# Kernel optimization log

Measured on AMD Instinct MI355X. Metric: run time of the kernel, lower is better.

Reference implementation:

```python
import math
import jax, jax.numpy as jnp
import numpy as np

E = 1024          # emb_size
H = 16            # num_heads
D = E // H        # head_dim
B, S = 4, 2048
DI = 64           # intent dim
K = 32            # num intent clusters
ASSIGN_W = 0.5
MU_W = 0.5
UNC_W = 0.5
EXPLORE_SCALE = 0.5
EXPLOIT_SCALE = 0.5
TEMP_MIN = 0.5
TEMP_MAX = 2.0


def setup_inputs() -> dict:
    key = jax.random.key(0)
    ks = jax.random.split(key, 16)
    inp = {
        "his_emb": jax.random.normal(ks[0], (B, S, E), dtype=jnp.float32),
        "src_key_padding_mask": jax.random.randint(ks[1], (B, S), 0, 2).astype(bool),
        "intent_mu": jax.random.normal(ks[2], (B, S, DI), dtype=jnp.float32),
        "intent_sigma": jax.random.uniform(ks[3], (B, S, DI), dtype=jnp.float32),
        "intent_assign": jax.random.uniform(ks[4], (B, S, K), dtype=jnp.float32),
        "explore": jax.random.uniform(ks[5], (B, S), dtype=jnp.float32),
        "exploit": jax.random.uniform(ks[6], (B, S), dtype=jnp.float32),
    }
    std = 0.02
    inp["Wq"] = jax.random.normal(ks[7], (E, E), dtype=jnp.float32) * std
    inp["bq"] = jnp.zeros((E,), dtype=jnp.float32)
    inp["Wk"] = jax.random.normal(ks[8], (E, E), dtype=jnp.float32) * std
    inp["bk"] = jnp.zeros((E,), dtype=jnp.float32)
    inp["Wv"] = jax.random.normal(ks[9], (E, E), dtype=jnp.float32) * std
    inp["bv"] = jnp.zeros((E,), dtype=jnp.float32)
    inp["Wo"] = jax.random.normal(ks[10], (E, E), dtype=jnp.float32) * std
    inp["bo"] = jnp.zeros((E,), dtype=jnp.float32)
    return inp


def _forward(his_emb, src_key_padding_mask, intent_mu, intent_sigma, intent_assign,
             explore, exploit, Wq, bq, Wk, bk, Wv, bv, Wo, bo):
    b, s, _ = his_emb.shape
    # projections -> [b, h, s, d]
    def proj(W, bias):
        return (his_emb @ W.T + bias).reshape(b, s, H, D).transpose(0, 2, 1, 3)
    q, k, v = proj(Wq, bq), proj(Wk, bk), proj(Wv, bv)

    logits = jnp.einsum("bhqd,bhkd->bhqk", q, k) / math.sqrt(D)  # [b,h,s,s]

    # intent bias [b, s, s]
    assign_sim = jnp.einsum("bqc,bkc->bqk", intent_assign, intent_assign)
    bias = ASSIGN_W * assign_sim
    # mean squared distance via expansion (avoids [b,s,s,DI] intermediate)
    sq = jnp.sum(intent_mu * intent_mu, axis=-1)  # [b,s]
    dot = jnp.einsum("bqd,bkd->bqk", intent_mu, intent_mu)
    mu_dist = (sq[:, :, None] + sq[:, None, :] - 2.0 * dot) / DI
    bias = bias - MU_W * mu_dist
    uncertainty = jnp.mean(intent_sigma, axis=-1)[:, None, :]  # [b,1,s] over keys
    bias = bias - UNC_W * uncertainty

    logits = logits + bias[:, None, :, :]

    attn_mask = src_key_padding_mask[:, None, None, :]  # [b,1,1,s]
    logits = jnp.where(attn_mask, -1e16, logits)

    # per-query temperature scaling
    temperature = 1.0 + EXPLORE_SCALE * explore - EXPLOIT_SCALE * exploit
    temperature = jnp.clip(temperature, TEMP_MIN, TEMP_MAX)
    temperature = jnp.where(src_key_padding_mask, 1.0, temperature)  # [b,s]
    logits = logits / temperature[:, None, :, None]

    probs = jax.nn.softmax(logits, axis=-1)
    probs = jnp.where(attn_mask, 0.0, probs)
    probs = probs / jnp.maximum(jnp.sum(probs, axis=-1, keepdims=True), 1e-8)

    out = jnp.einsum("bhqk,bhkd->bhqd", probs, v)
    out = out.transpose(0, 2, 1, 3).reshape(b, s, E)
    out = out @ Wo.T + bo
    return jnp.where(src_key_padding_mask[:, :, None], 0.0, out)


def reference(his_emb, src_key_padding_mask, intent_mu, intent_sigma, intent_assign,
              explore, exploit, Wq, bq, Wk, bk, Wv, bv, Wo, bo):
    return _forward(his_emb, src_key_padding_mask, intent_mu, intent_sigma,
                    intent_assign, explore, exploit, Wq, bq, Wk, bk, Wv, bv, Wo, bo)
```

## Files before the change

kernel.cpp:

```cpp
#include <hip/hip_runtime.h>
#include <hip/hip_bf16.h>
#include <stdint.h>
#include <stddef.h>

#define Bn 4
#define Sn 2048
#define En 1024
#define Hn 16
#define DIn 64
#define BSn (Bn*Sn)
#define L2E 1.44269504089f
#define SH8L 11.5415603271f

typedef __attribute__((ext_vector_type(8))) short short8;
typedef __attribute__((ext_vector_type(4))) short short4v;
typedef __attribute__((ext_vector_type(4))) float fx4;
typedef __attribute__((ext_vector_type(16))) float fx16;
typedef __attribute__((ext_vector_type(8))) _Float16 half8;
typedef __attribute__((ext_vector_type(2))) __fp16 fp16x2;
typedef __attribute__((ext_vector_type(4))) int ix4;

__device__ __forceinline__ short f2bf(float f){
  union U { __hip_bfloat16 h; short s; } u; u.h = __float2bfloat16(f); return u.s;
}
__device__ __forceinline__ short f2h(float f){
  _Float16 h = (_Float16)f; return __builtin_bit_cast(short, h);
}

__device__ __forceinline__ void async16(const void* g, void* l){
  __builtin_amdgcn_global_load_lds((const __attribute__((address_space(1))) unsigned int*)g,
                                   (__attribute__((address_space(3))) unsigned int*)l, 16, 0, 0);
}

__device__ __forceinline__ fx4 mfma_bf(short8 a, short8 b, fx4 c){
  return __builtin_amdgcn_mfma_f32_16x16x32_bf16(a, b, c, 0, 0, 0);
}
__device__ __forceinline__ fx4 mfma_h(short8 a, short8 b, fx4 c){
  return __builtin_amdgcn_mfma_f32_16x16x32_f16(__builtin_bit_cast(half8, a),
                                                __builtin_bit_cast(half8, b), c, 0, 0, 0);
}
__device__ __forceinline__ fx16 mfma32h(short8 a, short8 b, fx16 c){
  return __builtin_amdgcn_mfma_f32_32x32x16_f16(__builtin_bit_cast(half8, a),
                                                __builtin_bit_cast(half8, b), c, 0, 0, 0);
}

#define FENCE asm volatile("" ::: "memory")
#define WAIT_VM4 asm volatile("s_waitcnt vmcnt(4)" ::: "memory")
#define WAIT_VM8 asm volatile("s_waitcnt vmcnt(8)" ::: "memory")
#define WAIT_VM0 asm volatile("s_waitcnt vmcnt(0)" ::: "memory")
#define WAIT_LGKM0 asm volatile("s_waitcnt lgkmcnt(0)" ::: "memory")

__global__ void scan_mask_k(const int* __restrict__ mask, int* __restrict__ sidx,
                            int* __restrict__ scnt){
  int b = blockIdx.x;
  const int* mb = mask + (size_t)b*Sn;
  __shared__ int wsum[4];
  int tid = threadIdx.x;
  int v[8]; int c = 0;
  #pragma unroll
  for (int j=0;j<8;j++){ v[j] = (mb[tid*8+j] == 0); c += v[j]; }
  int lane = tid&63, wv = tid>>6;
  int pref = c;
  #pragma unroll
  for (int m=1; m<64; m<<=1){ int o = __shfl_up(pref, m, 64); if (lane >= m) pref += o; }
  if (lane==63) wsum[wv] = pref;
  __syncthreads();
  int wbase = 0;
  for (int wprev=0; wprev<wv; wprev++) wbase += wsum[wprev];
  int pos = wbase + pref - c;
  #pragma unroll
  for (int j=0;j<8;j++){ if (v[j]) sidx[(size_t)b*Sn + pos++] = tid*8+j; }
  if (tid==255) scnt[b] = wbase + pref;
}

__global__ void prep_rows_k(const float* __restrict__ mu, const float* __restrict__ sigma,
                            const float* __restrict__ assign, const float* __restrict__ explore,
                            const float* __restrict__ exploit, const int* __restrict__ mask,
                            _Float16* __restrict__ F, _Float16* __restrict__ G,
                            float* __restrict__ a1L){
  int r = blockIdx.x*4 + (threadIdx.x>>6);
  int lane = threadIdx.x & 63;
  float muv = mu[(size_t)r*DIn + lane];
  float sgv = sigma[(size_t)r*DIn + lane];
  float sq = muv*muv, sg = sgv;
  #pragma unroll
  for (int m=32; m; m>>=1){ sq += __shfl_xor(sq,m,64); sg += __shfl_xor(sg,m,64); }
  float unc = sg*(1.f/64.f);
  #pragma unroll
  for (int cb=0; cb<128; cb+=64){
    int col = cb + lane;
    float fv, gv;
    if (col < 32){ float a = assign[(size_t)r*32 + col]; fv = 0.5f*a; gv = a; }
    else if (col < 96){ float m2 = mu[(size_t)r*DIn + (col-32)]; fv = m2*(1.f/64.f); gv = m2; }
    else if (col == 96){ fv = -sq*(1.f/128.f); gv = 1.f; }
    else if (col == 97){ fv = 1.f; gv = -(sq*(1.f/128.f) + 0.5f*unc); }
    else { fv = 0.f; gv = 0.f; }
    F[(size_t)r*128 + col] = (_Float16)fv;
    G[(size_t)r*128 + col] = (_Float16)gv;
  }
  if (lane == 0){
    int mk = mask[r];
    float t = 1.f + 0.5f*explore[r] - 0.5f*exploit[r];
    t = fminf(fmaxf(t, 0.5f), 2.f);
    if (mk) t = 1.f;
    a1L[r] = 0.125f/t * L2E;
  }
}

__global__ __launch_bounds__(256) void gather_x_k(
    const float* __restrict__ his, const int* __restrict__ sidx, const int* __restrict__ scnt,
    const float* __restrict__ a1L, short* __restrict__ Xc, float* __restrict__ a1Lc)
{
  int b = blockIdx.y, jb = blockIdx.x;
  int cnt = scnt[b];
  int scp = (cnt + 127) & ~127;
  int j0 = jb*64;
  if (j0 >= scp) return;
  __shared__ int sj[64];
  int tid = threadIdx.x;
  if (tid < 64){
    int j = j0 + tid;
    int s = (j < cnt) ? sidx[(size_t)b*Sn + j] : -1;
    sj[tid] = s;
    a1Lc[(size_t)b*Sn + j] = (s >= 0) ? a1L[(size_t)b*Sn + s] : 1.0f;
  }
  __syncthreads();
  const float* hb = his + (size_t)b*Sn*En;
  short* Xb_ = Xc + ((size_t)b*Sn + j0)*En;
  #pragma unroll 4
  for (int it=0; it<64; it++){
    int i = it*256 + tid;
    int r = i>>8, c = i&255;
    int s = sj[r];
    short4v o;
    if (s >= 0){
      fx4 v = *(const fx4*)(hb + (size_t)s*En + c*4);
      o = (short4v){ f2bf(v[0]), f2bf(v[1]), f2bf(v[2]), f2bf(v[3]) };
    } else o = (short4v){0,0,0,0};
    *(short4v*)(Xb_ + (size_t)r*En + c*4) = o;
  }
}

__global__ void cast_w_k(const float* __restrict__ Wq, const float* __restrict__ Wk,
                         const float* __restrict__ Wv, const float* __restrict__ Wo,
                         short* __restrict__ WQKV, short* __restrict__ Wof){
  int i = blockIdx.x*256 + threadIdx.x;
  int seg = i >> 18;
  int off = i & 262143;
  const float* src = (seg==0)?Wq:(seg==1)?Wk:(seg==2)?Wv:Wo;
  fx4 v = ((const fx4*)src)[off];
  short4v o;
  if (seg < 3) o = (short4v){ f2bf(v[0]), f2bf(v[1]), f2bf(v[2]), f2bf(v[3]) };
  else         o = (short4v){ f2h(v[0]),  f2h(v[1]),  f2h(v[2]),  f2h(v[3])  };
  if (seg < 3) ((short4v*)WQKV)[(size_t)seg*262144 + off] = o;
  else         ((short4v*)Wof)[off] = o;
}

__global__ void zero_masked_k(const int* __restrict__ mask, float* __restrict__ out){
  int row = blockIdx.x;
  if (!mask[row]) return;
  fx4 z = {0.f,0.f,0.f,0.f};
  ((fx4*)(out + (size_t)row*En))[threadIdx.x] = z;
}


__global__ __launch_bounds__(256) void gemm_qkv_k(
    const short* __restrict__ A, const short* __restrict__ Wqkv,
    short* __restrict__ Q, short* __restrict__ K, short* __restrict__ Vt,
    const float* __restrict__ bq, const float* __restrict__ bk, const float* __restrict__ bv,
    const int* __restrict__ scnt)
{
  __shared__ short sm[17408];
  short* Ct = sm;
  const int tid = threadIdx.x;
  const int wv = tid>>6, lane = tid&63, quad = lane>>4, l16 = lane&15;
  const int m0 = blockIdx.y*128, n0g = blockIdx.x*128;
  const int bb = m0 >> 11, jloc = m0 & 2047;
  const int scp = (scnt[bb] + 127) & ~127;
  if (jloc >= scp) return;
  const int seg = n0g >> 10, nloc = n0g & 1023;
  const int wm = (wv>>1)*64, wn = (wv&1)*64;
  int srw[2], sgc[2];
  #pragma unroll
  for (int i=0; i<2; i++){
    int idx = i*256 + tid;
    srw[i] = 2*(idx>>3) + (idx&1);
    sgc[i] = (((idx>>1)&3) ^ ((idx>>3)&3))*8;
  }
  auto stage = [&](int kt, short* dA, short* dB){
    int k0 = kt*32;
    #pragma unroll
    for (int i=0; i<2; i++){
      int idx = i*256 + tid;
      async16(A    + (size_t)(m0+srw[i])*En  + k0 + sgc[i], dA + idx*8);
      async16(Wqkv + (size_t)(n0g+srw[i])*En + k0 + sgc[i], dB + idx*8);
    }
  };
  fx4 acc[4][4] = {};
  int roffA[4], roffB[4];
  #pragma unroll
  for (int mi=0; mi<4; mi++){
    int row = wm + mi*16 + l16;
    roffA[mi] = (row>>1)*64 + ((quad ^ ((row>>1)&3))*16) + (row&1)*8;
    int rowb = wn + mi*16 + l16;
    roffB[mi] = (rowb>>1)*64 + ((quad ^ ((rowb>>1)&3))*16) + (rowb&1)*8;
  }
  auto compute = [&](const short* cA, const short* cB){
    short8 af[4], bfr[4];
    #pragma unroll
    for (int mi=0; mi<4; mi++) af[mi]  = *(const short8*)&cA[roffA[mi]];
    #pragma unroll
    for (int ni=0; ni<4; ni++) bfr[ni] = *(const short8*)&cB[roffB[ni]];
    #pragma unroll
    for (int mi=0; mi<4; mi++)
      #pragma unroll
      for (int ni=0; ni<4; ni++)
        acc[mi][ni] = mfma_bf(af[mi], bfr[ni], acc[mi][ni]);
  };
  stage(0, sm, sm+8192);
  for (int kt2=0; kt2<16; kt2++){
    stage(2*kt2+1, sm+4096, sm+12288);
    WAIT_VM4;
    __builtin_amdgcn_s_barrier(); FENCE;
    compute(sm, sm+8192);
    WAIT_LGKM0;
    __builtin_amdgcn_s_barrier(); FENCE;
    if (kt2 < 15){ stage(2*kt2+2, sm, sm+8192); WAIT_VM4; }
    else         { WAIT_VM0; }
    __builtin_amdgcn_s_barrier(); FENCE;
    compute(sm+4096, sm+12288);
    WAIT_LGKM0;
    __builtin_amdgcn_s_barrier(); FENCE;
  }
  __syncthreads();
  const float* biasv = (seg == 0) ? bq : (seg == 1) ? bk : bv;
  if (seg < 2){
    short* C = seg ? K : Q;
    #pragma unroll
    for (int mi=0; mi<4; mi++)
      #pragma unroll
      for (int ni=0; ni<4; ni++){
        int col = nloc + wn + ni*16 + l16;
        float b0 = biasv[col];
        #pragma unroll
        for (int rg=0; rg<4; rg++){
          int row = m0 + wm + mi*16 + quad*4 + rg;
          C[(size_t)row*En + col] = f2h(acc[mi][ni][rg] + b0);
        }
      }
  } else {
    #pragma unroll
    for (int mi=0; mi<4; mi++)
      #pragma unroll
      for (int ni=0; ni<4; ni++){
        int lcol = wn + ni*16 + l16;
        int lrow = wm + mi*16 + quad*4;
        float b0 = biasv[nloc + lcol];
        short4v pk;
        #pragma unroll
        for (int rg=0; rg<4; rg++) pk[rg] = f2h(acc[mi][ni][rg] + b0);
        *(short4v*)&Ct[lcol*136 + lrow] = pk;
      }
    __syncthreads();
    int sl = (tid&15)*8;
    #pragma unroll
    for (int e8=0; e8<8; e8++){
      int e_l = e8*16 + (tid>>4);
      fx4 val = *(const fx4*)&Ct[e_l*136 + sl];
      int e_g = nloc + e_l;
      size_t dst = ((size_t)(bb*Hn + (e_g>>6))*64 + (e_g&63))*Sn + jloc + sl;
      *(fx4*)&Vt[dst] = val;
    }
  }
}

__global__ __launch_bounds__(256) void gemm_bias_k(
    const short* __restrict__ G, const short* __restrict__ F, _Float16* __restrict__ biasT,
    const float* __restrict__ a1Lc, const int* __restrict__ sidx, const int* __restrict__ scnt)
{
  __shared__ short sm[32768];
  const int tid = threadIdx.x, b = blockIdx.z;
  const int cnt = scnt[b];
  const int scp64  = (cnt + 63) & ~63;
  const int scp128 = (cnt + 127) & ~127;
  const int m0 = blockIdx.y*128, n0 = blockIdx.x*128;
  if (m0 >= scp64)  return;
  if (n0 >= scp128) return;
  const int wv = tid>>6, lane = tid&63, quad = lane>>4, l16 = lane&15;
  const int wm = (wv>>1)*64, wn = (wv&1)*64;
  const short* Gb = G + (size_t)b*Sn*128;
  const short* Fb = F + (size_t)b*Sn*128;
  const int* sx = sidx + (size_t)b*Sn;
  int rA[4], rB[4];
  #pragma unroll
  for (int i=0; i<4; i++){
    int s = i*256 + tid;
    int r = s>>3;
    int gr = m0 + r;  rA[i] = (gr < cnt) ? sx[gr] : 0;
    int qr = n0 + r;  rB[i] = (qr < cnt) ? sx[qr] : 0;
  }
  #pragma unroll
  for (int h=0; h<2; h++){
    #pragma unroll
    for (int i=0; i<4; i++){
      int s = i*256 + tid;
      int r = s>>3, cl8 = s&7;
      int cg = (h*8 + (cl8 ^ (r&7)))*8;
      async16(Gb + (size_t)rA[i]*128 + cg, &sm[h*8192 + s*8]);
      async16(Fb + (size_t)rB[i]*128 + cg, &sm[16384 + h*8192 + s*8]);
    }
  }
  fx4 acc[4][4] = {};
  #pragma unroll
  for (int h=0; h<2; h++){
    if (h == 0){ WAIT_VM8; } else { WAIT_VM0; }
    __builtin_amdgcn_s_barrier();
    FENCE;
    #pragma unroll
    for (int kk=0; kk<2; kk++){
      short8 af[4], bfr[4];
      #pragma unroll
      for (int mi=0; mi<4; mi++){
        int row = wm + mi*16 + l16, pc = (kk*4+quad) ^ (row&7);
        af[mi] = *(const short8*)&sm[h*8192 + row*64 + pc*8];
      }
      #pragma unroll
      for (int ni=0; ni<4; ni++){
        int row = wn + ni*16 + l16, pc = (kk*4+quad) ^ (row&7);
        bfr[ni] = *(const short8*)&sm[16384 + h*8192 + row*64 + pc*8];
      }
      #pragma unroll
      for (int mi=0; mi<4; mi++)
        #pragma unroll
        for (int ni=0; ni<4; ni++)
          acc[mi][ni] = mfma_h(af[mi], bfr[ni], acc[mi][ni]);
    }
  }
  _Float16* bQ = biasT + (size_t)b*Sn*Sn;
  #pragma unroll
  for (int mi=0; mi<4; mi++)
    #pragma unroll
    for (int ni=0; ni<4; ni++){
      int col = n0 + wn + ni*16 + l16;
      int rowb = m0 + wm + mi*16 + quad*4;
      float s8 = 8.f * a1Lc[b*Sn + col];
      short4v pk;
      #pragma unroll
      for (int rg=0; rg<4; rg++){
        int s = rowb + rg;
        short hv;
        if (s >= cnt) hv = (short)0xFC00;
        else hv = f2h(acc[mi][ni][rg]*s8 - SH8L);
        pk[rg] = hv;
      }
      *(short4v*)&bQ[((size_t)(rowb>>3)*Sn + col)*8 + (rowb&7)] = pk;
    }
}

__global__ __launch_bounds__(256) void gemm_out_k(
    const short* __restrict__ A, const short* __restrict__ Bm, float* __restrict__ C,
    const float* __restrict__ biasv, const int* __restrict__ sidx, const int* __restrict__ scnt)
{
  __shared__ short sm[16384];
  const int tid = threadIdx.x;
  const int wv = tid>>6, lane = tid&63, quad = lane>>4, l16 = lane&15;
  const int m0 = blockIdx.y*128, n0 = blockIdx.x*128;
  const int b = m0 >> 11, jloc = m0 & 2047;
  const int cnt = scnt[b];
  const int scp = (cnt + 127) & ~127;
  if (jloc >= scp) return;
  const int* sx = sidx + (size_t)b*Sn;
  const int wm = (wv>>1)*64, wn = (wv&1)*64;
  int srw[2], sgc[2];
  #pragma unroll
  for (int i=0; i<2; i++){
    int idx = i*256 + tid;
    srw[i] = 2*(idx>>3) + (idx&1);
    sgc[i] = (((idx>>1)&3) ^ ((idx>>3)&3))*8;
  }
  auto stage = [&](int kt, short* dA, short* dB){
    int k0 = kt*32;
    #pragma unroll
    for (int i=0; i<2; i++){
      int idx = i*256 + tid;
      async16(A  + (size_t)(m0+srw[i])*En + k0 + sgc[i], dA + idx*8);
      async16(Bm + (size_t)(n0+srw[i])*En + k0 + sgc[i], dB + idx*8);
    }
  };
  fx4 acc[4][4] = {};
  int roffA[4], roffB[4];
  #pragma unroll
  for (int mi=0; mi<4; mi++){
    int row = wm + mi*16 + l16;
    roffA[mi] = (row>>1)*64 + ((quad ^ ((row>>1)&3))*16) + (row&1)*8;
    int rowb = wn + mi*16 + l16;
    roffB[mi] = (rowb>>1)*64 + ((quad ^ ((rowb>>1)&3))*16) + (rowb&1)*8;
  }
  auto compute = [&](const short* cA, const short* cB){
    short8 af[4], bfr[4];
    #pragma unroll
    for (int mi=0; mi<4; mi++) af[mi]  = *(const short8*)&cA[roffA[mi]];
    #pragma unroll
    for (int ni=0; ni<4; ni++) bfr[ni] = *(const short8*)&cB[roffB[ni]];
    #pragma unroll
    for (int mi=0; mi<4; mi++)
      #pragma unroll
      for (int ni=0; ni<4; ni++)
        acc[mi][ni] = mfma_h(af[mi], bfr[ni], acc[mi][ni]);
  };
  stage(0, sm, sm+8192);
  for (int kt2=0; kt2<16; kt2++){
    stage(2*kt2+1, sm+4096, sm+12288);
    WAIT_VM4;
    __builtin_amdgcn_s_barrier(); FENCE;
    compute(sm, sm+8192);
    WAIT_LGKM0;
    __builtin_amdgcn_s_barrier(); FENCE;
    if (kt2 < 15){ stage(2*kt2+2, sm, sm+8192); WAIT_VM4; }
    else         { WAIT_VM0; }
    __builtin_amdgcn_s_barrier(); FENCE;
    compute(sm+4096, sm+12288);
    WAIT_LGKM0;
    __builtin_amdgcn_s_barrier(); FENCE;
  }
  #pragma unroll
  for (int mi=0; mi<4; mi++)
    #pragma unroll
    for (int ni=0; ni<4; ni++)
      #pragma unroll
      for (int rg=0; rg<4; rg++){
        int j = jloc + wm + mi*16 + quad*4 + rg;
        if (j < cnt){
          int row = b*Sn + sx[j];
          int col = n0 + wn + ni*16 + l16;
          C[(size_t)row*En + col] = acc[mi][ni][rg] + biasv[col];
        }
      }
}

__global__ __launch_bounds__(256, 4) void flash7_k(
    const short* __restrict__ Qg, const short* __restrict__ Kg, const short* __restrict__ Vtg,
    const _Float16* __restrict__ biasB, const float* __restrict__ a1Lv,
    const int* __restrict__ scnt, short* __restrict__ AO)
{
  __shared__ short smem[2][2][64*64];
  const int tid = threadIdx.x, wv = tid>>6, lane = tid&63;
  const int l32 = lane&31, hi = lane>>5;
  const int q0 = blockIdx.x*128;
  const int b = blockIdx.y >> 4, h = blockIdx.y & 15;
  const int cnt = scnt[b];
  const int NT = ((cnt + 63) & ~63) >> 6;
  const int scp128 = (cnt + 127) & ~127;
  if (q0 >= scp128) return;
  const short* Qb  = Qg  + (size_t)b*Sn*En + h*64;
  const int q = q0 + wv*32 + l32;
  const float a1L = a1Lv[b*Sn + q];

  const int r0 = tid>>3, c0 = (tid&7) ^ (r0&7);
  const int kr0 = (r0 & 51) | ((r0&4)<<1) | ((r0&8)>>1);
  const short* kA = Kg  + (size_t)b*Sn*En + h*64 + (size_t)kr0*En + c0*8;
  const short* vA = Vtg + (size_t)(b*Hn + h)*64*Sn + (size_t)r0*Sn + c0*8;
  const _Float16* bP = biasB + (size_t)b*Sn*Sn + ((size_t)hi*Sn + q)*8;
  const int ld0 = tid*8;

  auto issue = [&](int buf){
    short* base = &smem[buf][0][0];
    async16(kA,             base + ld0);
    async16(kA + 32*En,     base + 2048 + ld0);
    async16(vA,             base + 4096 + ld0);
    async16(vA + 32*Sn,     base + 4096 + 2048 + ld0);
  };
  if (NT > 0){ issue(0); }
  kA += 64*En; vA += 64;

  short8 qf[4];
  #pragma unroll
  for (int c=0; c<4; c++)
    qf[c] = *(const short8*)(Qb + (size_t)q*En + c*16 + hi*8);

  int koff[2][4], voff[2][4];
  #pragma unroll
  for (int t=0; t<2; t++){
    int m = t*32 + l32;
    #pragma unroll
    for (int c=0; c<4; c++)
      koff[t][c] = m*64 + (((c*2 + hi) ^ (m&7))*8);
  }
  #pragma unroll
  for (int ds=0; ds<2; ds++){
    int rv = ds*32 + l32;
    #pragma unroll
    for (int sc=0; sc<4; sc++)
      voff[ds][sc] = 4096 + rv*64 + (((sc*2 + hi) ^ (rv&7))*8);
  }

  fp16x2 one2; one2[0] = (__fp16)1.0f; one2[1] = (__fp16)1.0f;
  fx16 o0 = {}, o1 = {};
  float psum = 0.f;

  for (int T=0; T<NT; T++){
    __syncthreads();
    const short* base = &smem[T&1][0][0];
    if (T < NT-1){ issue((T&1)^1); kA += 64*En; vA += 64; }

    #pragma unroll
    for (int t=0; t<2; t++){
      half8 bch[2];
      #pragma unroll
      for (int c2=0; c2<2; c2++)
        bch[c2] = *(const half8*)(bP + (size_t)(t*4 + c2*2)*Sn*8);
      fx16 sa = {};
      #pragma unroll
      for (int c=0; c<4; c++){
        short8 ka = *(const short8*)(base + koff[t][c]);
        sa = mfma32h(ka, qf[c], sa);
      }
      #pragma unroll
      for (int c2=0; c2<2; c2++){
        fp16x2 pk_[4];
        #pragma unroll
        for (int jj=0; jj<4; jj++){
          float pa = __builtin_amdgcn_exp2f(fmaf(sa[c2*8 + jj*2],     a1L, (float)bch[c2][jj*2]));
          float pb = __builtin_amdgcn_exp2f(fmaf(sa[c2*8 + jj*2 + 1], a1L, (float)bch[c2][jj*2+1]));
          pk_[jj] = __builtin_amdgcn_cvt_pkrtz(pa, pb);
          psum = __builtin_amdgcn_fdot2(pk_[jj], one2, psum, false);
        }
        ix4 fr = { __builtin_bit_cast(int, pk_[0]), __builtin_bit_cast(int, pk_[1]),
                   __builtin_bit_cast(int, pk_[2]), __builtin_bit_cast(int, pk_[3]) };
        short8 pfr = __builtin_bit_cast(short8, fr);
        int sc = t*2 + c2;
        #pragma unroll
        for (int ds=0; ds<2; ds++){
          short8 va = *(const short8*)(base + voff[ds][sc]);
          if (ds == 0) o0 = mfma32h(va, pfr, o0);
          else         o1 = mfma32h(va, pfr, o1);
        }
      }
    }
    bP += (size_t)8*Sn*8;
  }

  psum += __shfl_xor(psum, 32, 64);
  float linv = 1.f/fmaxf(psum, 1e-30f);

  __syncthreads();
  short* stage = &smem[0][0][0] + wv*2304;
  #pragma unroll
  for (int ds=0; ds<2; ds++){
    const fx16& o = ds ? o1 : o0;
    #pragma unroll
    for (int rq=0; rq<4; rq++){
      int d0 = ds*32 + rq*8 + hi*4;
      short4v pk;
      #pragma unroll
      for (int j=0; j<4; j++) pk[j] = f2h(o[rq*4 + j]*linv);
      *(short4v*)&stage[l32*72 + d0] = pk;
    }
  }
  short* AOb = AO + (size_t)b*Sn*En + h*64;
  #pragma unroll
  for (int rnd=0; rnd<4; rnd++){
    int idx = rnd*64 + lane;
    int r = idx>>3, ch = idx&7;
    fx4 val = *(const fx4*)&stage[r*72 + ch*8];
    *(fx4*)(AOb + (size_t)(q0 + wv*32 + r)*En + ch*8) = val;
  }
}

extern "C" void kernel_launch(void* const* d_in, const int* in_sizes, int n_in,
                              void* d_out, int out_size, void* d_ws, size_t ws_size,
                              hipStream_t stream)
{
  const float* his     = (const float*)d_in[0];
  const int*   mask    = (const int*)  d_in[1];
  const float* mu      = (const float*)d_in[2];
  const float* sigma   = (const float*)d_in[3];
  const float* assign  = (const float*)d_in[4];
  const float* explore = (const float*)d_in[5];
  const float* exploit = (const float*)d_in[6];
  const float* Wq = (const float*)d_in[7];  const float* bq = (const float*)d_in[8];
  const float* Wk = (const float*)d_in[9];  const float* bk = (const float*)d_in[10];
  const float* Wv = (const float*)d_in[11]; const float* bv = (const float*)d_in[12];
  const float* Wo = (const float*)d_in[13]; const float* bo = (const float*)d_in[14];

  char* w = (char*)d_ws;
  size_t off = 0;
  auto alloc = [&](size_t bytes){ void* p = w + off; off += (bytes + 255) & ~(size_t)255; return p; };
  short*     Xc    = (short*)alloc((size_t)BSn*En*2);
  short*     WQKV  = (short*)alloc((size_t)3*En*En*2);
  short*     Wof   = (short*)alloc((size_t)En*En*2);
  short*     Qc    = (short*)alloc((size_t)BSn*En*2);
  short*     Kc    = (short*)alloc((size_t)BSn*En*2);
  short*     Vtc   = (short*)alloc((size_t)BSn*En*2);
  short*     AO    = (short*)alloc((size_t)BSn*En*2);
  _Float16*  F     = (_Float16*)alloc((size_t)BSn*128*2);
  _Float16*  G     = (_Float16*)alloc((size_t)BSn*128*2);
  _Float16*  biasT = (_Float16*)alloc((size_t)Bn*Sn*Sn*2);
  float*     a1Lp  = (float*)alloc((size_t)BSn*4);
  float*     a1Lc  = (float*)alloc((size_t)BSn*4);
  int*       sidx  = (int*)alloc((size_t)BSn*4);
  int*       scnt  = (int*)alloc(256);
  (void)ws_size; (void)in_sizes; (void)n_in; (void)out_size;

  scan_mask_k<<<Bn, 256, 0, stream>>>(mask, sidx, scnt);
  prep_rows_k<<<BSn/4, 256, 0, stream>>>(mu, sigma, assign, explore, exploit, mask, F, G, a1Lp);
  cast_w_k<<<4*En*En/4/256, 256, 0, stream>>>(Wq, Wk, Wv, Wo, WQKV, Wof);
  gather_x_k<<<dim3(Sn/64, Bn), 256, 0, stream>>>(his, sidx, scnt, a1Lp, Xc, a1Lc);
  zero_masked_k<<<BSn, 256, 0, stream>>>(mask, (float*)d_out);
  gemm_qkv_k<<<dim3(3*En/128, BSn/128), 256, 0, stream>>>(Xc, WQKV, Qc, Kc, Vtc, bq, bk, bv, scnt);
  gemm_bias_k<<<dim3(Sn/128, Sn/128, Bn), 256, 0, stream>>>(
      (const short*)G, (const short*)F, biasT, a1Lc, sidx, scnt);
  flash7_k<<<dim3(Sn/128, Bn*Hn), 256, 0, stream>>>(Qc, Kc, Vtc, biasT, a1Lc, scnt, AO);
  gemm_out_k<<<dim3(En/128, BSn/128), 256, 0, stream>>>(AO, Wof, (float*)d_out, bo, sidx, scnt);
}
```

Measured before the change: 285.1 us.

## Merge prep kernels and co-schedule QKV and bias GEMMs in one launch

Four small preprocessing kernels (weight cast, row gather, row prep, masked-row zeroing) are merged into one launch whose block ranges dispatch to each task. The temperature scale is now computed inline during the gather instead of through an intermediate buffer. The QKV projection GEMM and the intent-bias GEMM are combined into one kernel with interleaved block indices (3 QKV tiles per 2 bias tiles) and launch_bounds occupancy 4. The bias GEMM is rewritten to use the same double-buffered staging layout as the QKV GEMM. This removes launch gaps and lets the two independent GEMMs fill the GPU together, at the cost of divergent block roles and register pressure set by the larger branch.

```diff
diff --git a/kernel.cpp b/kernel.cpp
--- a/kernel.cpp
+++ b/kernel.cpp
@@ -46,7 +46,6 @@
 
 #define FENCE asm volatile("" ::: "memory")
 #define WAIT_VM4 asm volatile("s_waitcnt vmcnt(4)" ::: "memory")
-#define WAIT_VM8 asm volatile("s_waitcnt vmcnt(8)" ::: "memory")
 #define WAIT_VM0 asm volatile("s_waitcnt vmcnt(0)" ::: "memory")
 #define WAIT_LGKM0 asm volatile("s_waitcnt lgkmcnt(0)" ::: "memory")
 
@@ -73,113 +72,108 @@
   if (tid==255) scnt[b] = wbase + pref;
 }
 
-__global__ void prep_rows_k(const float* __restrict__ mu, const float* __restrict__ sigma,
-                            const float* __restrict__ assign, const float* __restrict__ explore,
-                            const float* __restrict__ exploit, const int* __restrict__ mask,
-                            _Float16* __restrict__ F, _Float16* __restrict__ G,
-                            float* __restrict__ a1L){
-  int r = blockIdx.x*4 + (threadIdx.x>>6);
-  int lane = threadIdx.x & 63;
-  float muv = mu[(size_t)r*DIn + lane];
-  float sgv = sigma[(size_t)r*DIn + lane];
-  float sq = muv*muv, sg = sgv;
-  #pragma unroll
-  for (int m=32; m; m>>=1){ sq += __shfl_xor(sq,m,64); sg += __shfl_xor(sg,m,64); }
-  float unc = sg*(1.f/64.f);
-  #pragma unroll
-  for (int cb=0; cb<128; cb+=64){
-    int col = cb + lane;
-    float fv, gv;
-    if (col < 32){ float a = assign[(size_t)r*32 + col]; fv = 0.5f*a; gv = a; }
-    else if (col < 96){ float m2 = mu[(size_t)r*DIn + (col-32)]; fv = m2*(1.f/64.f); gv = m2; }
-    else if (col == 96){ fv = -sq*(1.f/128.f); gv = 1.f; }
-    else if (col == 97){ fv = 1.f; gv = -(sq*(1.f/128.f) + 0.5f*unc); }
-    else { fv = 0.f; gv = 0.f; }
-    F[(size_t)r*128 + col] = (_Float16)fv;
-    G[(size_t)r*128 + col] = (_Float16)gv;
-  }
-  if (lane == 0){
-    int mk = mask[r];
-    float t = 1.f + 0.5f*explore[r] - 0.5f*exploit[r];
-    t = fminf(fmaxf(t, 0.5f), 2.f);
-    if (mk) t = 1.f;
-    a1L[r] = 0.125f/t * L2E;
-  }
-}
-
-__global__ __launch_bounds__(256) void gather_x_k(
+__global__ __launch_bounds__(256) void fused_prep_k(
     const float* __restrict__ his, const int* __restrict__ sidx, const int* __restrict__ scnt,
-    const float* __restrict__ a1L, short* __restrict__ Xc, float* __restrict__ a1Lc)
+    const float* __restrict__ mu, const float* __restrict__ sigma,
+    const float* __restrict__ assign, const float* __restrict__ explore,
+    const float* __restrict__ exploit, const int* __restrict__ mask,
+    const float* __restrict__ Wq, const float* __restrict__ Wk,
+    const float* __restrict__ Wv, const float* __restrict__ Wo,
+    short* __restrict__ WQKV, short* __restrict__ Wof,
+    short* __restrict__ Xc, float* __restrict__ a1Lc,
+    _Float16* __restrict__ F, _Float16* __restrict__ G, float* __restrict__ out)
 {
-  int b = blockIdx.y, jb = blockIdx.x;
-  int cnt = scnt[b];
-  int scp = (cnt + 127) & ~127;
-  int j0 = jb*64;
-  if (j0 >= scp) return;
   __shared__ int sj[64];
-  int tid = threadIdx.x;
-  if (tid < 64){
-    int j = j0 + tid;
-    int s = (j < cnt) ? sidx[(size_t)b*Sn + j] : -1;
-    sj[tid] = s;
-    a1Lc[(size_t)b*Sn + j] = (s >= 0) ? a1L[(size_t)b*Sn + s] : 1.0f;
-  }
-  __syncthreads();
-  const float* hb = his + (size_t)b*Sn*En;
-  short* Xb_ = Xc + ((size_t)b*Sn + j0)*En;
-  #pragma unroll 4
-  for (int it=0; it<64; it++){
-    int i = it*256 + tid;
-    int r = i>>8, c = i&255;
-    int s = sj[r];
+  const int id = blockIdx.x, tid = threadIdx.x;
+  if (id < 4096){
+    int i = id*256 + tid;
+    int seg = i >> 18;
+    int off = i & 262143;
+    const float* src = (seg==0)?Wq:(seg==1)?Wk:(seg==2)?Wv:Wo;
+    fx4 v = ((const fx4*)src)[off];
     short4v o;
-    if (s >= 0){
-      fx4 v = *(const fx4*)(hb + (size_t)s*En + c*4);
-      o = (short4v){ f2bf(v[0]), f2bf(v[1]), f2bf(v[2]), f2bf(v[3]) };
-    } else o = (short4v){0,0,0,0};
-    *(short4v*)(Xb_ + (size_t)r*En + c*4) = o;
-  }
-}
-
-__global__ void cast_w_k(const float* __restrict__ Wq, const float* __restrict__ Wk,
-                         const float* __restrict__ Wv, const float* __restrict__ Wo,
-                         short* __restrict__ WQKV, short* __restrict__ Wof){
-  int i = blockIdx.x*256 + threadIdx.x;
-  int seg = i >> 18;
-  int off = i & 262143;
-  const float* src = (seg==0)?Wq:(seg==1)?Wk:(seg==2)?Wv:Wo;
-  fx4 v = ((const fx4*)src)[off];
-  short4v o;
-  if (seg < 3) o = (short4v){ f2bf(v[0]), f2bf(v[1]), f2bf(v[2]), f2bf(v[3]) };
-  else         o = (short4v){ f2h(v[0]),  f2h(v[1]),  f2h(v[2]),  f2h(v[3])  };
-  if (seg < 3) ((short4v*)WQKV)[(size_t)seg*262144 + off] = o;
-  else         ((short4v*)Wof)[off] = o;
-}
-
-__global__ void zero_masked_k(const int* __restrict__ mask, float* __restrict__ out){
-  int row = blockIdx.x;
-  if (!mask[row]) return;
-  fx4 z = {0.f,0.f,0.f,0.f};
-  ((fx4*)(out + (size_t)row*En))[threadIdx.x] = z;
-}
-
-
-__global__ __launch_bounds__(256) void gemm_qkv_k(
+    if (seg < 3) o = (short4v){ f2bf(v[0]), f2bf(v[1]), f2bf(v[2]), f2bf(v[3]) };
+    else         o = (short4v){ f2h(v[0]),  f2h(v[1]),  f2h(v[2]),  f2h(v[3])  };
+    if (seg < 3) ((short4v*)WQKV)[(size_t)seg*262144 + off] = o;
+    else         ((short4v*)Wof)[off] = o;
+  } else if (id < 4224){
+    int t = id - 4096;
+    int b = t >> 5, jb = t & 31;
+    int cnt = scnt[b];
+    int scp = (cnt + 127) & ~127;
+    int j0 = jb*64;
+    if (j0 >= scp) return;
+    if (tid < 64){
+      int j = j0 + tid;
+      int s = (j < cnt) ? sidx[(size_t)b*Sn + j] : -1;
+      sj[tid] = s;
+      float a1 = 1.0f;
+      if (s >= 0){
+        float tt = 1.f + 0.5f*explore[(size_t)b*Sn + s] - 0.5f*exploit[(size_t)b*Sn + s];
+        tt = fminf(fmaxf(tt, 0.5f), 2.f);
+        a1 = 0.125f/tt * L2E;
+      }
+      a1Lc[(size_t)b*Sn + j] = a1;
+    }
+    __syncthreads();
+    const float* hb = his + (size_t)b*Sn*En;
+    short* Xb_ = Xc + ((size_t)b*Sn + j0)*En;
+    #pragma unroll 4
+    for (int it=0; it<64; it++){
+      int i = it*256 + tid;
+      int r = i>>8, c = i&255;
+      int s = sj[r];
+      short4v o;
+      if (s >= 0){
+        fx4 v = *(const fx4*)(hb + (size_t)s*En + c*4);
+        o = (short4v){ f2bf(v[0]), f2bf(v[1]), f2bf(v[2]), f2bf(v[3]) };
+      } else o = (short4v){0,0,0,0};
+      *(short4v*)(Xb_ + (size_t)r*En + c*4) = o;
+    }
+  } else {
+    int r = (id - 4224)*4 + (tid>>6);
+    int lane = tid & 63;
+    float muv = mu[(size_t)r*DIn + lane];
+    float sgv = sigma[(size_t)r*DIn + lane];
+    float sq = muv*muv, sg = sgv;
+    #pragma unroll
+    for (int m=32; m; m>>=1){ sq += __shfl_xor(sq,m,64); sg += __shfl_xor(sg,m,64); }
+    float unc = sg*(1.f/64.f);
+    #pragma unroll
+    for (int cb=0; cb<128; cb+=64){
+      int col = cb + lane;
+      float fv, gv;
+      if (col < 32){ float a = assign[(size_t)r*32 + col]; fv = 0.5f*a; gv = a; }
+      else if (col < 96){ float m2 = mu[(size_t)r*DIn + (col-32)]; fv = m2*(1.f/64.f); gv = m2; }
+      else if (col == 96){ fv = -sq*(1.f/128.f); gv = 1.f; }
+      else if (col == 97){ fv = 1.f; gv = -(sq*(1.f/128.f) + 0.5f*unc); }
+      else { fv = 0.f; gv = 0.f; }
+      F[(size_t)r*128 + col] = (_Float16)fv;
+      G[(size_t)r*128 + col] = (_Float16)gv;
+    }
+    if (mask[r]){
+      fx4 z = {0.f,0.f,0.f,0.f};
+      #pragma unroll
+      for (int i2=0; i2<4; i2++)
+        ((fx4*)(out + (size_t)r*En))[lane + 64*i2] = z;
+    }
+  }
+}
+
+
+__global__ __launch_bounds__(256, 4) void fused_gemm_k(
     const short* __restrict__ A, const short* __restrict__ Wqkv,
     short* __restrict__ Q, short* __restrict__ K, short* __restrict__ Vt,
     const float* __restrict__ bq, const float* __restrict__ bk, const float* __restrict__ bv,
-    const int* __restrict__ scnt)
+    const _Float16* __restrict__ G, const _Float16* __restrict__ F,
+    _Float16* __restrict__ biasT, const float* __restrict__ a1Lc,
+    const int* __restrict__ sidx, const int* __restrict__ scnt)
 {
   __shared__ short sm[17408];
-  short* Ct = sm;
   const int tid = threadIdx.x;
   const int wv = tid>>6, lane = tid&63, quad = lane>>4, l16 = lane&15;
-  const int m0 = blockIdx.y*128, n0g = blockIdx.x*128;
-  const int bb = m0 >> 11, jloc = m0 & 2047;
-  const int scp = (scnt[bb] + 127) & ~127;
-  if (jloc >= scp) return;
-  const int seg = n0g >> 10, nloc = n0g & 1023;
   const int wm = (wv>>1)*64, wn = (wv&1)*64;
+  const int gid = blockIdx.x, g5 = gid/5, r5 = gid%5;
   int srw[2], sgc[2];
   #pragma unroll
   for (int i=0; i<2; i++){
@@ -187,16 +181,6 @@
     srw[i] = 2*(idx>>3) + (idx&1);
     sgc[i] = (((idx>>1)&3) ^ ((idx>>3)&3))*8;
   }
-  auto stage = [&](int kt, short* dA, short* dB){
-    int k0 = kt*32;
-    #pragma unroll
-    for (int i=0; i<2; i++){
-      int idx = i*256 + tid;
-      async16(A    + (size_t)(m0+srw[i])*En  + k0 + sgc[i], dA + idx*8);
-      async16(Wqkv + (size_t)(n0g+srw[i])*En + k0 + sgc[i], dB + idx*8);
-    }
-  };
-  fx4 acc[4][4] = {};
   int roffA[4], roffB[4];
   #pragma unroll
   for (int mi=0; mi<4; mi++){
@@ -205,156 +189,169 @@
     int rowb = wn + mi*16 + l16;
     roffB[mi] = (rowb>>1)*64 + ((quad ^ ((rowb>>1)&3))*16) + (rowb&1)*8;
   }
-  auto compute = [&](const short* cA, const short* cB){
-    short8 af[4], bfr[4];
-    #pragma unroll
-    for (int mi=0; mi<4; mi++) af[mi]  = *(const short8*)&cA[roffA[mi]];
-    #pragma unroll
-    for (int ni=0; ni<4; ni++) bfr[ni] = *(const short8*)&cB[roffB[ni]];
-    #pragma unroll
-    for (int mi=0; mi<4; mi++)
-      #pragma unroll
-      for (int ni=0; ni<4; ni++)
-        acc[mi][ni] = mfma_bf(af[mi], bfr[ni], acc[mi][ni]);
-  };
-  stage(0, sm, sm+8192);
-  for (int kt2=0; kt2<16; kt2++){
-    stage(2*kt2+1, sm+4096, sm+12288);
-    WAIT_VM4;
-    __builtin_amdgcn_s_barrier(); FENCE;
-    compute(sm, sm+8192);
-    WAIT_LGKM0;
-    __builtin_amdgcn_s_barrier(); FENCE;
-    if (kt2 < 15){ stage(2*kt2+2, sm, sm+8192); WAIT_VM4; }
-    else         { WAIT_VM0; }
-    __builtin_amdgcn_s_barrier(); FENCE;
-    compute(sm+4096, sm+12288);
-    WAIT_LGKM0;
-    __builtin_amdgcn_s_barrier(); FENCE;
-  }
-  __syncthreads();
-  const float* biasv = (seg == 0) ? bq : (seg == 1) ? bk : bv;
-  if (seg < 2){
-    short* C = seg ? K : Q;
-    #pragma unroll
-    for (int mi=0; mi<4; mi++)
-      #pragma unroll
-      for (int ni=0; ni<4; ni++){
-        int col = nloc + wn + ni*16 + l16;
-        float b0 = biasv[col];
+  short* A0 = sm;       short* A1 = sm + 4096;
+  short* B0 = sm + 8192; short* B1 = sm + 12288;
+  fx4 acc[4][4] = {};
+
+  if (r5 < 3){
+    int qi = g5*3 + r5;
+    const int m0 = (qi/24)*128, n0g = (qi%24)*128;
+    const int bb = m0 >> 11, jloc = m0 & 2047;
+    const int scp = (scnt[bb] + 127) & ~127;
+    if (jloc >= scp) return;
+    const int seg = n0g >> 10, nloc = n0g & 1023;
+    short* Ct = sm;
+    auto stage = [&](int kt, short* dA, short* dB){
+      int k0 = kt*32;
+      #pragma unroll
+      for (int i=0; i<2; i++){
+        int idx = i*256 + tid;
+        async16(A    + (size_t)(m0+srw[i])*En  + k0 + sgc[i], dA + idx*8);
+        async16(Wqkv + (size_t)(n0g+srw[i])*En + k0 + sgc[i], dB + idx*8);
+      }
+    };
+    auto compute = [&](const short* cA, const short* cB){
+      short8 af[4], bfr[4];
+      #pragma unroll
+      for (int mi=0; mi<4; mi++) af[mi]  = *(const short8*)&cA[roffA[mi]];
+      #pragma unroll
+      for (int ni=0; ni<4; ni++) bfr[ni] = *(const short8*)&cB[roffB[ni]];
+      #pragma unroll
+      for (int mi=0; mi<4; mi++)
         #pragma unroll
-        for (int rg=0; rg<4; rg++){
-          int row = m0 + wm + mi*16 + quad*4 + rg;
-          C[(size_t)row*En + col] = f2h(acc[mi][ni][rg] + b0);
+        for (int ni=0; ni<4; ni++)
+          acc[mi][ni] = mfma_bf(af[mi], bfr[ni], acc[mi][ni]);
+    };
+    stage(0, A0, B0);
+    for (int kt2=0; kt2<16; kt2++){
+      stage(2*kt2+1, A1, B1);
+      WAIT_VM4;
+      __builtin_amdgcn_s_barrier(); FENCE;
+      compute(A0, B0);
+      WAIT_LGKM0;
+      __builtin_amdgcn_s_barrier(); FENCE;
+      if (kt2 < 15){ stage(2*kt2+2, A0, B0); WAIT_VM4; }
+      else         { WAIT_VM0; }
+      __builtin_amdgcn_s_barrier(); FENCE;
+      compute(A1, B1);
+      WAIT_LGKM0;
+      __builtin_amdgcn_s_barrier(); FENCE;
+    }
+    __syncthreads();
+    const float* biasv = (seg == 0) ? bq : (seg == 1) ? bk : bv;
+    if (seg < 2){
+      short* C = seg ? K : Q;
+      #pragma unroll
+      for (int mi=0; mi<4; mi++)
+        #pragma unroll
+        for (int ni=0; ni<4; ni++){
+          int col = nloc + wn + ni*16 + l16;
+          float b0 = biasv[col];
+          #pragma unroll
+          for (int rg=0; rg<4; rg++){
+            int row = m0 + wm + mi*16 + quad*4 + rg;
+            C[(size_t)row*En + col] = f2h(acc[mi][ni][rg] + b0);
+          }
         }
-      }
+    } else {
+      #pragma unroll
+      for (int mi=0; mi<4; mi++)
+        #pragma unroll
+        for (int ni=0; ni<4; ni++){
+          int lcol = wn + ni*16 + l16;
+          int lrow = wm + mi*16 + quad*4;
+          float b0 = biasv[nloc + lcol];
+          short4v pk;
+          #pragma unroll
+          for (int rg=0; rg<4; rg++) pk[rg] = f2h(acc[mi][ni][rg] + b0);
+          *(short4v*)&Ct[lcol*136 + lrow] = pk;
+        }
+      __syncthreads();
+      int sl = (tid&15)*8;
+      #pragma unroll
+      for (int e8=0; e8<8; e8++){
+        int e_l = e8*16 + (tid>>4);
+        fx4 val = *(const fx4*)&Ct[e_l*136 + sl];
+        int e_g = nloc + e_l;
+        size_t dst = ((size_t)(bb*Hn + (e_g>>6))*64 + (e_g&63))*Sn + jloc + sl;
+        *(fx4*)&Vt[dst] = val;
+      }
+    }
   } else {
-    #pragma unroll
-    for (int mi=0; mi<4; mi++)
-      #pragma unroll
-      for (int ni=0; ni<4; ni++){
-        int lcol = wn + ni*16 + l16;
-        int lrow = wm + mi*16 + quad*4;
-        float b0 = biasv[nloc + lcol];
-        short4v pk;
-        #pragma unroll
-        for (int rg=0; rg<4; rg++) pk[rg] = f2h(acc[mi][ni][rg] + b0);
-        *(short4v*)&Ct[lcol*136 + lrow] = pk;
-      }
-    __syncthreads();
-    int sl = (tid&15)*8;
-    #pragma unroll
-    for (int e8=0; e8<8; e8++){
-      int e_l = e8*16 + (tid>>4);
-      fx4 val = *(const fx4*)&Ct[e_l*136 + sl];
-      int e_g = nloc + e_l;
-      size_t dst = ((size_t)(bb*Hn + (e_g>>6))*64 + (e_g&63))*Sn + jloc + sl;
-      *(fx4*)&Vt[dst] = val;
-    }
-  }
-}
-
-__global__ __launch_bounds__(256) void gemm_bias_k(
-    const short* __restrict__ G, const short* __restrict__ F, _Float16* __restrict__ biasT,
-    const float* __restrict__ a1Lc, const int* __restrict__ sidx, const int* __restrict__ scnt)
-{
-  __shared__ short sm[32768];
-  const int tid = threadIdx.x, b = blockIdx.z;
-  const int cnt = scnt[b];
-  const int scp64  = (cnt + 63) & ~63;
-  const int scp128 = (cnt + 127) & ~127;
-  const int m0 = blockIdx.y*128, n0 = blockIdx.x*128;
-  if (m0 >= scp64)  return;
-  if (n0 >= scp128) return;
-  const int wv = tid>>6, lane = tid&63, quad = lane>>4, l16 = lane&15;
-  const int wm = (wv>>1)*64, wn = (wv&1)*64;
-  const short* Gb = G + (size_t)b*Sn*128;
-  const short* Fb = F + (size_t)b*Sn*128;
-  const int* sx = sidx + (size_t)b*Sn;
-  int rA[4], rB[4];
-  #pragma unroll
-  for (int i=0; i<4; i++){
-    int s = i*256 + tid;
-    int r = s>>3;
-    int gr = m0 + r;  rA[i] = (gr < cnt) ? sx[gr] : 0;
-    int qr = n0 + r;  rB[i] = (qr < cnt) ? sx[qr] : 0;
-  }
-  #pragma unroll
-  for (int h=0; h<2; h++){
-    #pragma unroll
-    for (int i=0; i<4; i++){
-      int s = i*256 + tid;
-      int r = s>>3, cl8 = s&7;
-      int cg = (h*8 + (cl8 ^ (r&7)))*8;
-      async16(Gb + (size_t)rA[i]*128 + cg, &sm[h*8192 + s*8]);
-      async16(Fb + (size_t)rB[i]*128 + cg, &sm[16384 + h*8192 + s*8]);
-    }
-  }
-  fx4 acc[4][4] = {};
-  #pragma unroll
-  for (int h=0; h<2; h++){
-    if (h == 0){ WAIT_VM8; } else { WAIT_VM0; }
-    __builtin_amdgcn_s_barrier();
-    FENCE;
-    #pragma unroll
-    for (int kk=0; kk<2; kk++){
+    int bi = g5*2 + (r5-3);
+    const int b = bi >> 8, rem = bi & 255;
+    const int m0 = (rem >> 4)*128, n0 = (rem & 15)*128;
+    const int cnt = scnt[b];
+    const int scp64  = (cnt + 63) & ~63;
+    const int scp128 = (cnt + 127) & ~127;
+    if (m0 >= scp64)  return;
+    if (n0 >= scp128) return;
+    const short* Gb = (const short*)G + (size_t)b*Sn*128;
+    const short* Fb = (const short*)F + (size_t)b*Sn*128;
+    const int* sx = sidx + (size_t)b*Sn;
+    int rA[2], rB[2];
+    #pragma unroll
+    for (int i=0; i<2; i++){
+      int gr = m0 + srw[i];  rA[i] = (gr < cnt) ? sx[gr] : 0;
+      int qr = n0 + srw[i];  rB[i] = (qr < cnt) ? sx[qr] : 0;
+    }
+    auto stageB = [&](int kt, short* dA, short* dB){
+      int k0 = kt*32;
+      #pragma unroll
+      for (int i=0; i<2; i++){
+        int idx = i*256 + tid;
+        async16(Gb + (size_t)rA[i]*128 + k0 + sgc[i], dA + idx*8);
+        async16(Fb + (size_t)rB[i]*128 + k0 + sgc[i], dB + idx*8);
+      }
+    };
+    auto computeB = [&](const short* cA, const short* cB){
       short8 af[4], bfr[4];
       #pragma unroll
-      for (int mi=0; mi<4; mi++){
-        int row = wm + mi*16 + l16, pc = (kk*4+quad) ^ (row&7);
-        af[mi] = *(const short8*)&sm[h*8192 + row*64 + pc*8];
-      }
-      #pragma unroll
-      for (int ni=0; ni<4; ni++){
-        int row = wn + ni*16 + l16, pc = (kk*4+quad) ^ (row&7);
-        bfr[ni] = *(const short8*)&sm[16384 + h*8192 + row*64 + pc*8];
-      }
+      for (int mi=0; mi<4; mi++) af[mi]  = *(const short8*)&cA[roffA[mi]];
+      #pragma unroll
+      for (int ni=0; ni<4; ni++) bfr[ni] = *(const short8*)&cB[roffB[ni]];
       #pragma unroll
       for (int mi=0; mi<4; mi++)
         #pragma unroll
         for (int ni=0; ni<4; ni++)
           acc[mi][ni] = mfma_h(af[mi], bfr[ni], acc[mi][ni]);
-    }
-  }
-  _Float16* bQ = biasT + (size_t)b*Sn*Sn;
-  #pragma unroll
-  for (int mi=0; mi<4; mi++)
-    #pragma unroll
-    for (int ni=0; ni<4; ni++){
-      int col = n0 + wn + ni*16 + l16;
-      int rowb = m0 + wm + mi*16 + quad*4;
-      float s8 = 8.f * a1Lc[b*Sn + col];
-      short4v pk;
-      #pragma unroll
-      for (int rg=0; rg<4; rg++){
-        int s = rowb + rg;
-        short hv;
-        if (s >= cnt) hv = (short)0xFC00;
-        else hv = f2h(acc[mi][ni][rg]*s8 - SH8L);
-        pk[rg] = hv;
-      }
-      *(short4v*)&bQ[((size_t)(rowb>>3)*Sn + col)*8 + (rowb&7)] = pk;
-    }
+    };
+    stageB(0, A0, B0);
+    stageB(1, A1, B1); WAIT_VM4;
+    __builtin_amdgcn_s_barrier(); FENCE;
+    computeB(A0, B0); WAIT_LGKM0;
+    __builtin_amdgcn_s_barrier(); FENCE;
+    stageB(2, A0, B0); WAIT_VM4;
+    __builtin_amdgcn_s_barrier(); FENCE;
+    computeB(A1, B1); WAIT_LGKM0;
+    __builtin_amdgcn_s_barrier(); FENCE;
+    stageB(3, A1, B1); WAIT_VM4;
+    __builtin_amdgcn_s_barrier(); FENCE;
+    computeB(A0, B0); WAIT_LGKM0;
+    __builtin_amdgcn_s_barrier(); FENCE;
+    WAIT_VM0;
+    __builtin_amdgcn_s_barrier(); FENCE;
+    computeB(A1, B1);
+    _Float16* bQ = biasT + (size_t)b*Sn*Sn;
+    #pragma unroll
+    for (int mi=0; mi<4; mi++)
+      #pragma unroll
+      for (int ni=0; ni<4; ni++){
+        int col = n0 + wn + ni*16 + l16;
+        int rowb = m0 + wm + mi*16 + quad*4;
+        float s8 = 8.f * a1Lc[b*Sn + col];
+        short4v pk;
+        #pragma unroll
+        for (int rg=0; rg<4; rg++){
+          int s = rowb + rg;
+          short hv;
+          if (s >= cnt) hv = (short)0xFC00;
+          else hv = f2h(acc[mi][ni][rg]*s8 - SH8L);
+          pk[rg] = hv;
+        }
+        *(short4v*)&bQ[((size_t)(rowb>>3)*Sn + col)*8 + (rowb&7)] = pk;
+      }
+  }
 }
 
 __global__ __launch_bounds__(256) void gemm_out_k(
@@ -596,20 +593,18 @@
   _Float16*  F     = (_Float16*)alloc((size_t)BSn*128*2);
   _Float16*  G     = (_Float16*)alloc((size_t)BSn*128*2);
   _Float16*  biasT = (_Float16*)alloc((size_t)Bn*Sn*Sn*2);
-  float*     a1Lp  = (float*)alloc((size_t)BSn*4);
   float*     a1Lc  = (float*)alloc((size_t)BSn*4);
   int*       sidx  = (int*)alloc((size_t)BSn*4);
   int*       scnt  = (int*)alloc(256);
   (void)ws_size; (void)in_sizes; (void)n_in; (void)out_size;
 
   scan_mask_k<<<Bn, 256, 0, stream>>>(mask, sidx, scnt);
-  prep_rows_k<<<BSn/4, 256, 0, stream>>>(mu, sigma, assign, explore, exploit, mask, F, G, a1Lp);
-  cast_w_k<<<4*En*En/4/256, 256, 0, stream>>>(Wq, Wk, Wv, Wo, WQKV, Wof);
-  gather_x_k<<<dim3(Sn/64, Bn), 256, 0, stream>>>(his, sidx, scnt, a1Lp, Xc, a1Lc);
-  zero_masked_k<<<BSn, 256, 0, stream>>>(mask, (float*)d_out);
-  gemm_qkv_k<<<dim3(3*En/128, BSn/128), 256, 0, stream>>>(Xc, WQKV, Qc, Kc, Vtc, bq, bk, bv, scnt);
-  gemm_bias_k<<<dim3(Sn/128, Sn/128, Bn), 256, 0, stream>>>(
-      (const short*)G, (const short*)F, biasT, a1Lc, sidx, scnt);
+  fused_prep_k<<<6272, 256, 0, stream>>>(his, sidx, scnt, mu, sigma, assign, explore, exploit,
+                                         mask, Wq, Wk, Wv, Wo, WQKV, Wof, Xc, a1Lc, F, G,
+                                         (float*)d_out);
+  fused_gemm_k<<<2560, 256, 0, stream>>>(Xc, WQKV, Qc, Kc, Vtc, bq, bk, bv,
+                                         (const _Float16*)G, (const _Float16*)F,
+                                         biasT, a1Lc, sidx, scnt);
   flash7_k<<<dim3(Sn/128, Bn*Hn), 256, 0, stream>>>(Qc, Kc, Vtc, biasT, a1Lc, scnt, AO);
   gemm_out_k<<<dim3(En/128, BSn/128), 256, 0, stream>>>(AO, Wof, (float*)d_out, bo, sidx, scnt);
 }
```

New measurement: 273.8 us. 1.04x faster.
